# Kernel optimization log

Hardware: AMD Instinct MI355X
Metric: run time of the kernel (lower is better)

## Reference

```python
import jax, jax.numpy as jnp
import numpy as np

NUM_HEADS = 4
KEY_DIM = 64
D_MODEL = 256
OUTPUT_DIM = 256


def setup_inputs() -> dict:
    key = jax.random.key(0)
    ks = jax.random.split(key, 11)
    B, T, D = 16, 1024, D_MODEL
    HD = NUM_HEADS * KEY_DIM
    s = 0.02
    return {
        "query": jax.random.normal(ks[0], (B, T, D), jnp.float32),
        "key": jax.random.normal(ks[1], (B, T, D), jnp.float32),
        "value": jax.random.normal(ks[2], (B, T, D), jnp.float32),
        "Wq": jax.random.normal(ks[3], (D, HD), jnp.float32) * s,
        "bq": jnp.zeros((HD,), jnp.float32),
        "Wk": jax.random.normal(ks[4], (D, HD), jnp.float32) * s,
        "bk": jnp.zeros((HD,), jnp.float32),
        "Wv": jax.random.normal(ks[5], (D, KEY_DIM), jnp.float32) * s,
        "bv": jnp.zeros((KEY_DIM,), jnp.float32),
        "Wo": jax.random.normal(ks[6], (HD, OUTPUT_DIM), jnp.float32) * s,
        "bo": jnp.zeros((OUTPUT_DIM,), jnp.float32),
    }


def reference(query, key, value, Wq, bq, Wk, bk, Wv, bv, Wo, bo):
    B, Tq, _ = query.shape
    Tk = key.shape[1]
    H, Dk = NUM_HEADS, KEY_DIM
    # projections
    q = (query @ Wq + bq).reshape(B, Tq, H, Dk)  # [B,Tq,H,Dk]
    k = (key @ Wk + bk).reshape(B, Tk, H, Dk)    # [B,Tk,H,Dk]
    v = value @ Wv + bv                           # [B,Tk,Dk] shared across heads
    scale = jnp.asarray(Dk, q.dtype) ** -0.5
    # scores [B,H,Tq,Tk]
    score = jnp.einsum("bqhd,bkhd->bhqk", q, k) * scale
    attn = jax.nn.softmax(score, axis=-1)
    # broadcast-V attention: [B,H,Tq,Tk] x [B,Tk,Dk] -> [B,H,Tq,Dk]
    out = jnp.einsum("bhqk,bkd->bhqd", attn, v)
    out = out.transpose(0, 2, 1, 3).reshape(B, Tq, H * Dk)
    return out @ Wo + bo
```

## Files before the change

kernel.cpp:

```cpp
#include <hip/hip_runtime.h>
#include <hip/hip_bf16.h>


typedef __attribute__((ext_vector_type(8))) short short8;
typedef __attribute__((ext_vector_type(4))) short s16x4;
typedef __attribute__((ext_vector_type(4))) float f32x4;

__device__ __forceinline__ short f2bf(float x) {
    return __builtin_bit_cast(short, __float2bfloat16(x));
}

__device__ __forceinline__ float exp2_fast(float x) {
#if __has_builtin(__builtin_amdgcn_exp2f)
    return __builtin_amdgcn_exp2f(x);
#else
    float r; asm("v_exp_f32 %0, %1" : "=v"(r) : "v"(x)); return r;
#endif
}

__device__ __forceinline__ f32x4 mfma16(short8 a, short8 b, f32x4 c) {
    return __builtin_amdgcn_mfma_f32_16x16x32_bf16(a, b, c, 0, 0, 0);
}
__device__ __forceinline__ f32x4 mfma16k16(s16x4 a, s16x4 b, f32x4 c) {
    return __builtin_amdgcn_mfma_f32_16x16x16bf16_1k(a, b, c, 0, 0, 0);
}

__device__ __forceinline__ void gll16(const float4* gsrc, float4* ldst) {
    __builtin_amdgcn_global_load_lds(
        (const __attribute__((address_space(1))) void*)gsrc,
        (__attribute__((address_space(3))) void*)ldst, 16, 0, 0);
}

#define QSCALE 0.18033688011112042f

__global__ void prep_weights(const float* __restrict__ Wq, const float* __restrict__ Wk,
                             const float* __restrict__ Wv, const float* __restrict__ Wo,
                             short* __restrict__ WqtF, short* __restrict__ WktF,
                             short* __restrict__ WvtF, short* __restrict__ WotF) {
    int tid = blockIdx.x * 256 + threadIdx.x;
    int k = tid >> 8, n = tid & 255;
    int off = ((n >> 6) << 14) + (((n >> 4) & 3) << 12) + ((k >> 5) << 9)
            + (((k >> 3) & 3) << 7) + ((n & 15) << 3) + (k & 7);
    WqtF[off] = f2bf(Wq[k * 256 + n] * QSCALE);
    WktF[off] = f2bf(Wk[k * 256 + n]);
    WotF[off] = f2bf(Wo[k * 256 + n]);
    if (n < 64) {
        int offv = ((n >> 4) << 12) + ((k >> 5) << 9) + (((k >> 3) & 3) << 7)
                 + ((n & 15) << 3) + (k & 7);
        WvtF[offv] = f2bf(Wv[k * 64 + n]);
    }
}

__global__ __launch_bounds__(256) void proj_all(
        const float* __restrict__ query, const float* __restrict__ key_,
        const float* __restrict__ value,
        const short* __restrict__ WqtF, const short* __restrict__ WktF,
        const short* __restrict__ WvtF,
        const float* __restrict__ bq, const float* __restrict__ bk,
        const float* __restrict__ bv,
        short* __restrict__ qf, short* __restrict__ kf, short* __restrict__ vf) {
    __shared__ short At[8192];
    const int tid = threadIdx.x;
    const int lane = tid & 63, wave = tid >> 6;
    const int u = lane >> 4, r16 = lane & 15;
    const int m0 = blockIdx.x * 32;
    const int task = blockIdx.y;

    const float* A = task == 0 ? query : (task == 1 ? key_ : value);

    #pragma unroll
    for (int j = 0; j < 4; ++j) {
        int p8 = j * 8 + ((wave >> 1) << 2) + u;
        int row = ((wave & 1) << 4) + r16;
        const float* src = A + (m0 + row) * 256 + p8 * 8;
        float4 a0 = *(const float4*)src;
        float4 a1 = *(const float4*)(src + 4);
        short8 w;
        w[0] = f2bf(a0.x); w[1] = f2bf(a0.y); w[2] = f2bf(a0.z); w[3] = f2bf(a0.w);
        w[4] = f2bf(a1.x); w[5] = f2bf(a1.y); w[6] = f2bf(a1.z); w[7] = f2bf(a1.w);
        int dst = ((p8 >> 2) << 10) + ((wave & 1) << 9) + ((p8 & 3) << 7) + (r16 << 3);
        *(short8*)&At[dst] = w;
    }

    const int b = m0 >> 10, t64 = (m0 & 1023) >> 6, half = (m0 >> 5) & 1;

    if (task < 2) {
        const short* WtF = task == 0 ? WqtF : WktF;
        const float* bias = task == 0 ? bq : bk;
        const float bscale = task == 0 ? QSCALE : 1.0f;
        short* outF = task == 0 ? qf : kf;
        const short* wb = WtF + (wave << 14);

        short8 bf8[4];
        #pragma unroll
        for (int g = 0; g < 4; ++g) bf8[g] = *(const short8*)&wb[(g << 12) + lane * 8];
        __syncthreads();

        f32x4 acc[2][4] = {};
        #pragma unroll
        for (int kk = 0; kk < 8; ++kk) {
            short8 af[2], nb[4];
            #pragma unroll
            for (int f = 0; f < 2; ++f) af[f] = *(const short8*)&At[(kk << 10) + (f << 9) + lane * 8];
            if (kk < 7) {
                #pragma unroll
                for (int g = 0; g < 4; ++g) nb[g] = *(const short8*)&wb[(g << 12) + ((kk + 1) << 9) + lane * 8];
            }
            #pragma unroll
            for (int f = 0; f < 2; ++f)
                #pragma unroll
                for (int g = 0; g < 4; ++g)
                    acc[f][g] = mfma16(af[f], bf8[g], acc[f][g]);
            #pragma unroll
            for (int g = 0; g < 4; ++g) bf8[g] = nb[g];
        }

        float bvv[4];
        #pragma unroll
        for (int g = 0; g < 4; ++g) bvv[g] = bias[(wave << 6) + 16 * g + r16] * bscale;
        short* ob = outF + ((((b << 2) + wave) << 4) + t64) * 4096;
        #pragma unroll
        for (int f = 0; f < 2; ++f) {
            int fg = half * 2 + f;
            #pragma unroll
            for (int g = 0; g < 4; ++g) {
                int base = (fg << 10) + ((g >> 1) << 9)
                         + (((2 * g + (r16 >> 3)) & 3) << 7) + (r16 & 7);
                #pragma unroll
                for (int rr = 0; rr < 4; ++rr)
                    ob[base + (4 * u + rr) * 8] = f2bf(acc[f][g][rr] + bvv[g]);
            }
        }
    } else {
        const int f = wave >> 1;
        short8 bf8[2];
        #pragma unroll
        for (int z = 0; z < 2; ++z) {
            int dg = ((wave & 1) << 1) + z;
            bf8[z] = *(const short8*)&WvtF[(dg << 12) + lane * 8];
        }
        __syncthreads();

        f32x4 acc[2] = {};
        #pragma unroll
        for (int kk = 0; kk < 8; ++kk) {
            short8 af = *(const short8*)&At[(kk << 10) + (f << 9) + lane * 8];
            short8 nb[2];
            if (kk < 7) {
                #pragma unroll
                for (int z = 0; z < 2; ++z) {
                    int dg = ((wave & 1) << 1) + z;
                    nb[z] = *(const short8*)&WvtF[(dg << 12) + ((kk + 1) << 9) + lane * 8];
                }
            }
            #pragma unroll
            for (int z = 0; z < 2; ++z) acc[z] = mfma16(af, bf8[z], acc[z]);
            bf8[0] = nb[0]; bf8[1] = nb[1];
        }

        short* ob = vf + ((b << 4) + t64) * 4096;
        const int gg = half * 2 + f;
        #pragma unroll
        for (int z = 0; z < 2; ++z) {
            int dg = ((wave & 1) << 1) + z;
            float bvv = bv[16 * dg + r16];
            s16x4 o;
            #pragma unroll
            for (int rr = 0; rr < 4; ++rr) o[rr] = f2bf(acc[z][rr] + bvv);
            *(s16x4*)&ob[(dg << 10) + ((gg >> 1) << 9) + lane * 8 + ((gg & 1) << 2)] = o;
        }
    }
}

__global__ __launch_bounds__(512, 4) void attn_og(const short* __restrict__ qF,
        const short* __restrict__ kF, const short* __restrict__ vF,
        const short* __restrict__ WoF, const float* __restrict__ bo,
        float* __restrict__ outp) {
    __shared__ float4 KV3[3840];
    const int tid = threadIdx.x;
    const int lane = tid & 63, wave = tid >> 6;
    const int u = lane >> 4, r16 = lane & 15;
    const int h = wave & 3, qh = wave >> 2;

    const int L = (blockIdx.x & 7) * 64 + (blockIdx.x >> 3);
    const int b = L >> 5, qt = L & 31;

    const short* qb = qF + (((b << 2) + h) << 16) + ((qt >> 1) << 12);
    const int f64 = ((qt & 1) << 1) + qh;
    short8 qfr[2];
    #pragma unroll
    for (int c = 0; c < 2; ++c)
        qfr[c] = *(const short8*)&qb[(f64 << 10) + (c << 9) + lane * 8];

    #define STAGE(t, bufp)                                                          \
        {                                                                           \
            _Pragma("unroll")                                                       \
            for (int j_ = 0; j_ < 3; ++j_) {                                        \
                int ch_ = wave + 8 * j_;                                            \
                if (ch_ < 20) {                                                     \
                    const float4* src_;                                             \
                    if (ch_ < 16)                                                   \
                        src_ = (const float4*)kF + (((b << 2) + (ch_ >> 2)) * 8192) \
                             + (t) * 256 + ((ch_ & 3) << 6) + lane;                 \
                    else                                                            \
                        src_ = (const float4*)vF + (b * 8192) + ((t) >> 1) * 512    \
                             + ((ch_ - 16) << 7) + (((t) & 1) << 6) + lane;         \
                    gll16(src_, (bufp) + (ch_ << 6));                               \
                }                                                                   \
            }                                                                       \
        }

    float4* bc = KV3;
    float4* bn = KV3 + 1280;
    float4* bs = KV3 + 2560;

    STAGE(0, bc)
    STAGE(1, bn)
    asm volatile("s_waitcnt vmcnt(0)" ::: "memory");
    __builtin_amdgcn_s_barrier();

    f32x4 acc[4] = {};
    f32x4 accl = {};
    s16x4 ones;
    { short o = (short)0x3F80; ones[0] = o; ones[1] = o; ones[2] = o; ones[3] = o; }

    for (int kt = 0; kt < 32; ++kt) {
        if (kt < 30) STAGE(kt + 2, bs)

        const short* Kh = (const short*)bc + (h << 11);
        const short* Vb = (const short*)bc + 8192;

        short8 kf8[4];
        #pragma unroll
        for (int g = 0; g < 2; ++g)
            #pragma unroll
            for (int c = 0; c < 2; ++c)
                kf8[g * 2 + c] = *(const short8*)&Kh[(g << 10) + (c << 9) + lane * 8];

        f32x4 s[2];
        __builtin_amdgcn_s_setprio(1);
        #pragma unroll
        for (int g = 0; g < 2; ++g) {
            f32x4 z = {};
            z = mfma16(kf8[2 * g], qfr[0], z);
            s[g] = mfma16(kf8[2 * g + 1], qfr[1], z);
        }
        __builtin_amdgcn_s_setprio(0);

        s16x4 pk[2];
        #pragma unroll
        for (int g = 0; g < 2; ++g)
            #pragma unroll
            for (int rr = 0; rr < 4; ++rr)
                pk[g][rr] = f2bf(exp2_fast(s[g][rr]));

        __builtin_amdgcn_s_setprio(1);
        accl = mfma16k16(ones, pk[0], accl);
        accl = mfma16k16(ones, pk[1], accl);
        #pragma unroll
        for (int dg = 0; dg < 4; ++dg) {
            short8 v8 = *(const short8*)&Vb[(dg << 9) + lane * 8];
            s16x4 vlo = { v8[0], v8[1], v8[2], v8[3] };
            s16x4 vhi = { v8[4], v8[5], v8[6], v8[7] };
            acc[dg] = mfma16k16(vlo, pk[0], acc[dg]);
            acc[dg] = mfma16k16(vhi, pk[1], acc[dg]);
        }
        __builtin_amdgcn_s_setprio(0);

        if (kt < 30) {
            if (wave < 4) asm volatile("s_waitcnt vmcnt(3)" ::: "memory");
            else          asm volatile("s_waitcnt vmcnt(2)" ::: "memory");
            __builtin_amdgcn_s_barrier();
        } else if (kt == 30) {
            asm volatile("s_waitcnt vmcnt(0)" ::: "memory");
            __builtin_amdgcn_s_barrier();
        }
        float4* t_ = bc; bc = bn; bn = bs; bs = t_;
    }
    #undef STAGE

    __syncthreads();

    short* At = (short*)KV3;
    float linv = 1.0f / accl[0];
    #pragma unroll
    for (int dg = 0; dg < 4; ++dg) {
        s16x4 o;
        #pragma unroll
        for (int rr = 0; rr < 4; ++rr) o[rr] = f2bf(acc[dg][rr] * linv);
        int kk = 2 * h + (dg >> 1);
        int u2 = 2 * (dg & 1) + (u >> 1);
        int off = (kk << 10) + (qh << 9) + (u2 << 7) + (r16 << 3) + ((u & 1) << 2);
        *(s16x4*)&At[off] = o;
    }
    __syncthreads();

    const short* wb = WoF + ((wave >> 1) << 14) + ((wave & 1) << 13);
    f32x4 acc2[2][2] = {};
    #pragma unroll
    for (int kk = 0; kk < 8; ++kk) {
        short8 af[2], bf2[2];
        #pragma unroll
        for (int fq = 0; fq < 2; ++fq) af[fq] = *(const short8*)&At[(kk << 10) + (fq << 9) + lane * 8];
        #pragma unroll
        for (int gg = 0; gg < 2; ++gg) bf2[gg] = *(const short8*)&wb[(gg << 12) + (kk << 9) + lane * 8];
        #pragma unroll
        for (int fq = 0; fq < 2; ++fq)
            #pragma unroll
            for (int gg = 0; gg < 2; ++gg)
                acc2[fq][gg] = mfma16(af[fq], bf2[gg], acc2[fq][gg]);
    }

    const int m0 = L << 5;
    float bvv[2];
    #pragma unroll
    for (int gg = 0; gg < 2; ++gg) bvv[gg] = bo[(wave << 5) + (gg << 4) + r16];
    #pragma unroll
    for (int fq = 0; fq < 2; ++fq)
        #pragma unroll
        for (int gg = 0; gg < 2; ++gg)
            #pragma unroll
            for (int rr = 0; rr < 4; ++rr)
                outp[(m0 + 16 * fq + 4 * u + rr) * 256 + (wave << 5) + (gg << 4) + r16]
                    = acc2[fq][gg][rr] + bvv[gg];
}

extern "C" void kernel_launch(void* const* d_in, const int* in_sizes, int n_in,
                              void* d_out, int out_size, void* d_ws, size_t ws_size,
                              hipStream_t stream) {
    (void)in_sizes; (void)n_in; (void)out_size; (void)ws_size;
    const float* query = (const float*)d_in[0];
    const float* key_  = (const float*)d_in[1];
    const float* value = (const float*)d_in[2];
    const float* Wq = (const float*)d_in[3];
    const float* bq = (const float*)d_in[4];
    const float* Wk = (const float*)d_in[5];
    const float* bk = (const float*)d_in[6];
    const float* Wv = (const float*)d_in[7];
    const float* bv = (const float*)d_in[8];
    const float* Wo = (const float*)d_in[9];
    const float* bo = (const float*)d_in[10];
    float* outp = (float*)d_out;

    short* wsp  = (short*)d_ws;
    short* WqtF = wsp;
    short* WktF = wsp + 65536;
    short* WotF = wsp + 131072;
    short* WvtF = wsp + 196608;
    short* qf   = wsp + 212992;
    short* kf   = wsp + 4407296;
    short* vf   = wsp + 8601600;

    hipLaunchKernelGGL(prep_weights, dim3(256), dim3(256), 0, stream,
                       Wq, Wk, Wv, Wo, WqtF, WktF, WvtF, WotF);
    hipLaunchKernelGGL(proj_all, dim3(512, 3), dim3(256), 0, stream,
                       query, key_, value, WqtF, WktF, WvtF, bq, bk, bv, qf, kf, vf);
    hipLaunchKernelGGL(attn_og, dim3(512), dim3(512), 0, stream,
                       qf, kf, vf, WotF, bo, outp);
}
```

Before: 60.73 us.

## Rewrite attention with 32x32 MFMA tiles and register-resident K/V prefetch

Switches the attention kernel from 16x16 MFMA to 32x32x16 bf16 MFMA, with one wave per head covering 32 queries. K/V fragments are now loaded straight from global memory into registers with a one-tile prefetch, which drops the LDS triple-buffer and its barriers. The probability tile is converted in registers with cvt_pk_bf16 and permlane32_swap instead of LDS round trips, and the row sum is accumulated in scalar adds instead of a ones-MFMA. The projection and Wo layouts are rewritten to match the 32-wide fragments, and blocks shrink to 256 threads. This risks losing K/V sharing across waves through LDS, since each head's wave now reads global memory on its own, and it raises register pressure.

```diff
diff --git a/kernel.cpp b/kernel.cpp
--- a/kernel.cpp
+++ b/kernel.cpp
@@ -3,8 +3,8 @@
 
 
 typedef __attribute__((ext_vector_type(8))) short short8;
-typedef __attribute__((ext_vector_type(4))) short s16x4;
 typedef __attribute__((ext_vector_type(4))) float f32x4;
+typedef __attribute__((ext_vector_type(16))) float f32x16;
 
 __device__ __forceinline__ short f2bf(float x) {
     return __builtin_bit_cast(short, __float2bfloat16(x));
@@ -21,14 +21,27 @@
 __device__ __forceinline__ f32x4 mfma16(short8 a, short8 b, f32x4 c) {
     return __builtin_amdgcn_mfma_f32_16x16x32_bf16(a, b, c, 0, 0, 0);
 }
-__device__ __forceinline__ f32x4 mfma16k16(s16x4 a, s16x4 b, f32x4 c) {
-    return __builtin_amdgcn_mfma_f32_16x16x16bf16_1k(a, b, c, 0, 0, 0);
-}
-
-__device__ __forceinline__ void gll16(const float4* gsrc, float4* ldst) {
-    __builtin_amdgcn_global_load_lds(
-        (const __attribute__((address_space(1))) void*)gsrc,
-        (__attribute__((address_space(3))) void*)ldst, 16, 0, 0);
+__device__ __forceinline__ f32x16 mfma32(short8 a, short8 b, f32x16 c) {
+    return __builtin_amdgcn_mfma_f32_32x32x16_bf16(a, b, c, 0, 0, 0);
+}
+
+__device__ __forceinline__ int cvtpk(float lo, float hi) {
+    int r; asm("v_cvt_pk_bf16_f32 %0, %1, %2" : "=v"(r) : "v"(lo), "v"(hi));
+    return r;
+}
+__device__ __forceinline__ void swap32(int& a, int& b) {
+    asm("v_permlane32_swap_b32 %0, %1" : "+v"(a), "+v"(b));
+}
+
+__device__ __forceinline__ short8 half_frag(const f32x16& s, int base) {
+    int d0 = cvtpk(s[base + 0], s[base + 1]);
+    int d1 = cvtpk(s[base + 2], s[base + 3]);
+    int d2 = cvtpk(s[base + 4], s[base + 5]);
+    int d3 = cvtpk(s[base + 6], s[base + 7]);
+    swap32(d0, d2);
+    swap32(d1, d3);
+    int4 v = { d0, d1, d2, d3 };
+    return __builtin_bit_cast(short8, v);
 }
 
 #define QSCALE 0.18033688011112042f
@@ -43,7 +56,9 @@
             + (((k >> 3) & 3) << 7) + ((n & 15) << 3) + (k & 7);
     WqtF[off] = f2bf(Wq[k * 256 + n] * QSCALE);
     WktF[off] = f2bf(Wk[k * 256 + n]);
-    WotF[off] = f2bf(Wo[k * 256 + n]);
+    int offo = ((n >> 5) << 13) + ((k >> 4) << 9) + (((k & 15) >> 3) << 8)
+             + ((n & 31) << 3) + (k & 7);
+    WotF[offo] = f2bf(Wo[k * 256 + n]);
     if (n < 64) {
         int offv = ((n >> 4) << 12) + ((k >> 5) << 9) + (((k >> 3) & 3) << 7)
                  + ((n & 15) << 3) + (k & 7);
@@ -82,7 +97,7 @@
         *(short8*)&At[dst] = w;
     }
 
-    const int b = m0 >> 10, t64 = (m0 & 1023) >> 6, half = (m0 >> 5) & 1;
+    const int b = m0 >> 10, t32 = (m0 >> 5) & 31;
 
     if (task < 2) {
         const short* WtF = task == 0 ? WqtF : WktF;
@@ -118,21 +133,17 @@
         float bvv[4];
         #pragma unroll
         for (int g = 0; g < 4; ++g) bvv[g] = bias[(wave << 6) + 16 * g + r16] * bscale;
-        short* ob = outF + ((((b << 2) + wave) << 4) + t64) * 4096;
-        #pragma unroll
-        for (int f = 0; f < 2; ++f) {
-            int fg = half * 2 + f;
-            #pragma unroll
-            for (int g = 0; g < 4; ++g) {
-                int base = (fg << 10) + ((g >> 1) << 9)
-                         + (((2 * g + (r16 >> 3)) & 3) << 7) + (r16 & 7);
+        short* ob = outF + ((((b << 2) + wave) << 5) + t32) * 2048;
+        #pragma unroll
+        for (int f = 0; f < 2; ++f)
+            #pragma unroll
+            for (int g = 0; g < 4; ++g)
                 #pragma unroll
                 for (int rr = 0; rr < 4; ++rr)
-                    ob[base + (4 * u + rr) * 8] = f2bf(acc[f][g][rr] + bvv[g]);
-            }
-        }
+                    ob[(g << 9) + ((r16 >> 3) << 8) + (16 * f + 4 * u + rr) * 8 + (r16 & 7)]
+                        = f2bf(acc[f][g][rr] + bvv[g]);
     } else {
-        const int f = wave >> 1;
+        const int fr = wave >> 1;
         short8 bf8[2];
         #pragma unroll
         for (int z = 0; z < 2; ++z) {
@@ -144,7 +155,7 @@
         f32x4 acc[2] = {};
         #pragma unroll
         for (int kk = 0; kk < 8; ++kk) {
-            short8 af = *(const short8*)&At[(kk << 10) + (f << 9) + lane * 8];
+            short8 af = *(const short8*)&At[(kk << 10) + (fr << 9) + lane * 8];
             short8 nb[2];
             if (kk < 7) {
                 #pragma unroll
@@ -158,171 +169,130 @@
             bf8[0] = nb[0]; bf8[1] = nb[1];
         }
 
-        short* ob = vf + ((b << 4) + t64) * 4096;
-        const int gg = half * 2 + f;
+        short* ob = vf + ((b << 5) + t32) * 2048;
         #pragma unroll
         for (int z = 0; z < 2; ++z) {
             int dg = ((wave & 1) << 1) + z;
             float bvv = bv[16 * dg + r16];
-            s16x4 o;
-            #pragma unroll
-            for (int rr = 0; rr < 4; ++rr) o[rr] = f2bf(acc[z][rr] + bvv);
-            *(s16x4*)&ob[(dg << 10) + ((gg >> 1) << 9) + lane * 8 + ((gg & 1) << 2)] = o;
-        }
-    }
-}
-
-__global__ __launch_bounds__(512, 4) void attn_og(const short* __restrict__ qF,
+            #pragma unroll
+            for (int rr = 0; rr < 4; ++rr) {
+                int tl = 4 * u + rr;
+                ob[((dg >> 1) << 10) + (fr << 9) + ((tl >> 3) << 8)
+                   + ((16 * (dg & 1) + r16) << 3) + (tl & 7)]
+                    = f2bf(acc[z][rr] + bvv);
+            }
+        }
+    }
+}
+
+__global__ __launch_bounds__(256, 3) void attn_og(const short* __restrict__ qF,
         const short* __restrict__ kF, const short* __restrict__ vF,
         const short* __restrict__ WoF, const float* __restrict__ bo,
         float* __restrict__ outp) {
-    __shared__ float4 KV3[3840];
+    __shared__ short At[8192];
     const int tid = threadIdx.x;
-    const int lane = tid & 63, wave = tid >> 6;
-    const int u = lane >> 4, r16 = lane & 15;
-    const int h = wave & 3, qh = wave >> 2;
+    const int lane = tid & 63, h = tid >> 6;
+    const int u2 = lane >> 5, n31 = lane & 31;
 
     const int L = (blockIdx.x & 7) * 64 + (blockIdx.x >> 3);
     const int b = L >> 5, qt = L & 31;
 
-    const short* qb = qF + (((b << 2) + h) << 16) + ((qt >> 1) << 12);
-    const int f64 = ((qt & 1) << 1) + qh;
-    short8 qfr[2];
-    #pragma unroll
-    for (int c = 0; c < 2; ++c)
-        qfr[c] = *(const short8*)&qb[(f64 << 10) + (c << 9) + lane * 8];
-
-    #define STAGE(t, bufp)                                                          \
-        {                                                                           \
-            _Pragma("unroll")                                                       \
-            for (int j_ = 0; j_ < 3; ++j_) {                                        \
-                int ch_ = wave + 8 * j_;                                            \
-                if (ch_ < 20) {                                                     \
-                    const float4* src_;                                             \
-                    if (ch_ < 16)                                                   \
-                        src_ = (const float4*)kF + (((b << 2) + (ch_ >> 2)) * 8192) \
-                             + (t) * 256 + ((ch_ & 3) << 6) + lane;                 \
-                    else                                                            \
-                        src_ = (const float4*)vF + (b * 8192) + ((t) >> 1) * 512    \
-                             + ((ch_ - 16) << 7) + (((t) & 1) << 6) + lane;         \
-                    gll16(src_, (bufp) + (ch_ << 6));                               \
-                }                                                                   \
-            }                                                                       \
-        }
-
-    float4* bc = KV3;
-    float4* bn = KV3 + 1280;
-    float4* bs = KV3 + 2560;
-
-    STAGE(0, bc)
-    STAGE(1, bn)
-    asm volatile("s_waitcnt vmcnt(0)" ::: "memory");
-    __builtin_amdgcn_s_barrier();
-
-    f32x4 acc[4] = {};
-    f32x4 accl = {};
-    s16x4 ones;
-    { short o = (short)0x3F80; ones[0] = o; ones[1] = o; ones[2] = o; ones[3] = o; }
+    const short* qb = qF + ((((b << 2) + h) << 5) + qt) * 2048;
+    short8 Q[4];
+    #pragma unroll
+    for (int c = 0; c < 4; ++c) Q[c] = *(const short8*)&qb[(c << 9) + lane * 8];
+
+    const short* kb = kF + (((b << 2) + h) << 5) * 2048;
+    const short* vb = vF + (b << 5) * 2048;
+
+    short8 kfr[4], vfr[4];
+    #pragma unroll
+    for (int c = 0; c < 4; ++c) {
+        kfr[c] = *(const short8*)&kb[(c << 9) + lane * 8];
+        vfr[c] = *(const short8*)&vb[(c << 9) + lane * 8];
+    }
+
+    f32x16 accO0 = {}, accO1 = {};
+    float l = 0.f;
 
     for (int kt = 0; kt < 32; ++kt) {
-        if (kt < 30) STAGE(kt + 2, bs)
-
-        const short* Kh = (const short*)bc + (h << 11);
-        const short* Vb = (const short*)bc + 8192;
-
-        short8 kf8[4];
-        #pragma unroll
-        for (int g = 0; g < 2; ++g)
-            #pragma unroll
-            for (int c = 0; c < 2; ++c)
-                kf8[g * 2 + c] = *(const short8*)&Kh[(g << 10) + (c << 9) + lane * 8];
-
-        f32x4 s[2];
+        short8 nk[4], nv[4];
+        if (kt < 31) {
+            const short* kn = kb + (kt + 1) * 2048;
+            const short* vn = vb + (kt + 1) * 2048;
+            #pragma unroll
+            for (int c = 0; c < 4; ++c) {
+                nk[c] = *(const short8*)&kn[(c << 9) + lane * 8];
+                nv[c] = *(const short8*)&vn[(c << 9) + lane * 8];
+            }
+        }
+
+        f32x16 S = {};
         __builtin_amdgcn_s_setprio(1);
-        #pragma unroll
-        for (int g = 0; g < 2; ++g) {
-            f32x4 z = {};
-            z = mfma16(kf8[2 * g], qfr[0], z);
-            s[g] = mfma16(kf8[2 * g + 1], qfr[1], z);
-        }
+        S = mfma32(kfr[0], Q[0], S);
+        S = mfma32(kfr[1], Q[1], S);
+        S = mfma32(kfr[2], Q[2], S);
+        S = mfma32(kfr[3], Q[3], S);
         __builtin_amdgcn_s_setprio(0);
 
-        s16x4 pk[2];
-        #pragma unroll
-        for (int g = 0; g < 2; ++g)
-            #pragma unroll
-            for (int rr = 0; rr < 4; ++rr)
-                pk[g][rr] = f2bf(exp2_fast(s[g][rr]));
+        f32x16 E;
+        #pragma unroll
+        for (int j = 0; j < 16; ++j) E[j] = exp2_fast(S[j]);
+        l += (((E[0] + E[1]) + (E[2] + E[3])) + ((E[4] + E[5]) + (E[6] + E[7])))
+           + (((E[8] + E[9]) + (E[10] + E[11])) + ((E[12] + E[13]) + (E[14] + E[15])));
+
+        short8 p0 = half_frag(E, 0);
+        short8 p1 = half_frag(E, 8);
 
         __builtin_amdgcn_s_setprio(1);
-        accl = mfma16k16(ones, pk[0], accl);
-        accl = mfma16k16(ones, pk[1], accl);
-        #pragma unroll
-        for (int dg = 0; dg < 4; ++dg) {
-            short8 v8 = *(const short8*)&Vb[(dg << 9) + lane * 8];
-            s16x4 vlo = { v8[0], v8[1], v8[2], v8[3] };
-            s16x4 vhi = { v8[4], v8[5], v8[6], v8[7] };
-            acc[dg] = mfma16k16(vlo, pk[0], acc[dg]);
-            acc[dg] = mfma16k16(vhi, pk[1], acc[dg]);
-        }
+        accO0 = mfma32(vfr[0], p0, accO0);
+        accO0 = mfma32(vfr[1], p1, accO0);
+        accO1 = mfma32(vfr[2], p0, accO1);
+        accO1 = mfma32(vfr[3], p1, accO1);
         __builtin_amdgcn_s_setprio(0);
 
-        if (kt < 30) {
-            if (wave < 4) asm volatile("s_waitcnt vmcnt(3)" ::: "memory");
-            else          asm volatile("s_waitcnt vmcnt(2)" ::: "memory");
-            __builtin_amdgcn_s_barrier();
-        } else if (kt == 30) {
-            asm volatile("s_waitcnt vmcnt(0)" ::: "memory");
-            __builtin_amdgcn_s_barrier();
-        }
-        float4* t_ = bc; bc = bn; bn = bs; bs = t_;
-    }
-    #undef STAGE
-
+        #pragma unroll
+        for (int c = 0; c < 4; ++c) { kfr[c] = nk[c]; vfr[c] = nv[c]; }
+    }
+
+    l += __shfl_xor(l, 32);
+    float linv = 1.0f / l;
+
+    f32x16 O0, O1;
+    #pragma unroll
+    for (int j = 0; j < 16; ++j) { O0[j] = accO0[j] * linv; O1[j] = accO1[j] * linv; }
+    {
+        short8 a0 = half_frag(O0, 0), a1 = half_frag(O0, 8);
+        short8 a2 = half_frag(O1, 0), a3 = half_frag(O1, 8);
+        *(short8*)&At[((4 * h + 0) << 9) + lane * 8] = a0;
+        *(short8*)&At[((4 * h + 1) << 9) + lane * 8] = a1;
+        *(short8*)&At[((4 * h + 2) << 9) + lane * 8] = a2;
+        *(short8*)&At[((4 * h + 3) << 9) + lane * 8] = a3;
+    }
     __syncthreads();
 
-    short* At = (short*)KV3;
-    float linv = 1.0f / accl[0];
-    #pragma unroll
-    for (int dg = 0; dg < 4; ++dg) {
-        s16x4 o;
-        #pragma unroll
-        for (int rr = 0; rr < 4; ++rr) o[rr] = f2bf(acc[dg][rr] * linv);
-        int kk = 2 * h + (dg >> 1);
-        int u2 = 2 * (dg & 1) + (u >> 1);
-        int off = (kk << 10) + (qh << 9) + (u2 << 7) + (r16 << 3) + ((u & 1) << 2);
-        *(s16x4*)&At[off] = o;
-    }
-    __syncthreads();
-
-    const short* wb = WoF + ((wave >> 1) << 14) + ((wave & 1) << 13);
-    f32x4 acc2[2][2] = {};
-    #pragma unroll
-    for (int kk = 0; kk < 8; ++kk) {
-        short8 af[2], bf2[2];
-        #pragma unroll
-        for (int fq = 0; fq < 2; ++fq) af[fq] = *(const short8*)&At[(kk << 10) + (fq << 9) + lane * 8];
-        #pragma unroll
-        for (int gg = 0; gg < 2; ++gg) bf2[gg] = *(const short8*)&wb[(gg << 12) + (kk << 9) + lane * 8];
-        #pragma unroll
-        for (int fq = 0; fq < 2; ++fq)
-            #pragma unroll
-            for (int gg = 0; gg < 2; ++gg)
-                acc2[fq][gg] = mfma16(af[fq], bf2[gg], acc2[fq][gg]);
+    const short* wo0 = WoF + (2 * h) * 8192;
+    const short* wo1 = wo0 + 8192;
+    f32x16 acc2[2] = {};
+    #pragma unroll
+    for (int kc = 0; kc < 16; ++kc) {
+        short8 a = *(const short8*)&At[(kc << 9) + lane * 8];
+        short8 w0 = *(const short8*)&wo0[(kc << 9) + lane * 8];
+        short8 w1 = *(const short8*)&wo1[(kc << 9) + lane * 8];
+        acc2[0] = mfma32(a, w0, acc2[0]);
+        acc2[1] = mfma32(a, w1, acc2[1]);
     }
 
     const int m0 = L << 5;
-    float bvv[2];
-    #pragma unroll
-    for (int gg = 0; gg < 2; ++gg) bvv[gg] = bo[(wave << 5) + (gg << 4) + r16];
-    #pragma unroll
-    for (int fq = 0; fq < 2; ++fq)
-        #pragma unroll
-        for (int gg = 0; gg < 2; ++gg)
-            #pragma unroll
-            for (int rr = 0; rr < 4; ++rr)
-                outp[(m0 + 16 * fq + 4 * u + rr) * 256 + (wave << 5) + (gg << 4) + r16]
-                    = acc2[fq][gg][rr] + bvv[gg];
+    #pragma unroll
+    for (int nt2 = 0; nt2 < 2; ++nt2) {
+        float bvv = bo[(2 * h + nt2) * 32 + n31];
+        #pragma unroll
+        for (int r = 0; r < 16; ++r) {
+            int q = (r & 3) + 8 * (r >> 2) + 4 * u2;
+            outp[(m0 + q) * 256 + (2 * h + nt2) * 32 + n31] = acc2[nt2][r] + bvv;
+        }
+    }
 }
 
 extern "C" void kernel_launch(void* const* d_in, const int* in_sizes, int n_in,
@@ -355,6 +325,6 @@
                        Wq, Wk, Wv, Wo, WqtF, WktF, WvtF, WotF);
     hipLaunchKernelGGL(proj_all, dim3(512, 3), dim3(256), 0, stream,
                        query, key_, value, WqtF, WktF, WvtF, bq, bk, bv, qf, kf, vf);
-    hipLaunchKernelGGL(attn_og, dim3(512), dim3(512), 0, stream,
+    hipLaunchKernelGGL(attn_og, dim3(512), dim3(256), 0, stream,
                        qf, kf, vf, WotF, bo, outp);
 }
```

New measurement: 55.29 us. 9.0% less time.
